# Performance work log

Hardware: AMD Instinct MI355X
Metric: run time of the kernel (lower is better)

Reference implementation:

```python
import jax, jax.numpy as jnp
import numpy as np

N_NODES = 100000
N_EDGES = 1600000
IN_DIM = 128
HID = 64
OUT_DIM = 3


def _glorot(key, shape):
    fan_in, fan_out = shape[0], shape[1]
    std = (2.0 / (fan_in + fan_out)) ** 0.5
    return jax.random.normal(key, shape, jnp.float32) * std


def setup_inputs() -> dict:
    key = jax.random.key(0)
    ks = jax.random.split(key, 12)
    x = jax.random.normal(ks[0], (N_NODES, IN_DIM), jnp.float32)
    edge_index = jax.random.randint(ks[1], (2, N_EDGES), 0, N_NODES, dtype=jnp.int32)
    return {
        "x": x,
        "edge_index": edge_index,
        "W1": _glorot(ks[2], (IN_DIM, HID)), "b1": jnp.zeros((HID,), jnp.float32),
        "W2": _glorot(ks[3], (HID, HID)), "b2": jnp.zeros((HID,), jnp.float32),
        "W3": _glorot(ks[4], (HID, HID)), "b3": jnp.zeros((HID,), jnp.float32),
        "W4": _glorot(ks[5], (HID, HID // 2)), "b4": jnp.zeros((HID // 2,), jnp.float32),
        "Wh": _glorot(ks[6], (HID // 2, OUT_DIM)), "bh": jnp.zeros((OUT_DIM,), jnp.float32),
    }


def reference(x, edge_index, W1, b1, W2, b2, W3, b3, W4, b4, Wh, bh):
    n = x.shape[0]
    self_loops = jnp.arange(n, dtype=edge_index.dtype)
    src = jnp.concatenate([edge_index[0], self_loops])  # message sources j
    dst = jnp.concatenate([edge_index[1], self_loops])  # aggregation targets i
    # symmetric GCN normalization with self-loops: deg over targets (unit edge weights)
    deg = jax.ops.segment_sum(jnp.ones_like(dst, jnp.float32), dst, num_segments=n)
    dinv = jnp.where(deg > 0, jax.lax.rsqrt(deg), 0.0)
    norm = dinv[src] * dinv[dst]  # [E+N]

    def gcn(h, W, b):
        h = h @ W  # transform first (PyG GCNConv order)
        agg = jax.ops.segment_sum(h[src] * norm[:, None], dst, num_segments=n)
        return agg + b

    h = jax.nn.relu(gcn(x, W1, b1))   # dropout is identity in eval mode
    h = jax.nn.relu(gcn(h, W2, b2))
    h = jax.nn.relu(gcn(h, W3, b3))
    h = jax.nn.relu(gcn(h, W4, b4))
    return h @ Wh + bh  # [N, 3]
```

## Files before the change

kernel.cpp:

```cpp
#include <hip/hip_runtime.h>
#include <hip/hip_bf16.h>
#include <hip/hip_fp16.h>
#include <cstdint>


#define MAXD 512
#define EB   8192
#define PADSLACK 2048

typedef _Float16 half8v __attribute__((ext_vector_type(8)));
typedef _Float16 half2v __attribute__((ext_vector_type(2)));
typedef float    float4v __attribute__((ext_vector_type(4)));

#if defined(__has_builtin)
#if __has_builtin(__builtin_amdgcn_fdot2)
#define HAVE_FDOT2 1
#endif
#endif

__device__ __forceinline__ float fdot2f(half2v a, half2v b, float c) {
#ifdef HAVE_FDOT2
    return __builtin_amdgcn_fdot2(a, b, c, false);
#else
    return c + (float)a[0] * (float)b[0] + (float)a[1] * (float)b[1];
#endif
}

__device__ __forceinline__ void digit_base_scan(const int* __restrict__ totals,
                                                int ND, int* pairs, int* cbs) {
    const int t = threadIdx.x;
    const int e0 = 2 * t, e1 = 2 * t + 1;
    int v0 = (e0 < ND) ? totals[e0] : 0;
    int v1 = (e1 < ND) ? totals[e1] : 0;
    pairs[t] = v0 + v1;
    __syncthreads();
    for (int off = 1; off < 256; off <<= 1) {
        int x = (t >= off) ? pairs[t - off] : 0;
        __syncthreads();
        pairs[t] += x;
        __syncthreads();
    }
    int ep = pairs[t] - v0 - v1;
    cbs[e0] = ep;
    cbs[e1] = ep + v0;
    __syncthreads();
}

__device__ __forceinline__ void hist_body(const int* __restrict__ ei,
                                          int* __restrict__ histM, int E, int b) {
    __shared__ int hist[MAXD];
    const int tid = threadIdx.x;
    hist[tid] = 0; hist[tid + 256] = 0;
    __syncthreads();
    const int base = b * EB;
#pragma unroll 2
    for (int it = 0; it < EB / 256; it += 4) {
        int d[4]; bool ok[4];
#pragma unroll
        for (int u = 0; u < 4; ++u) {
            int e = base + (it + u) * 256 + tid;
            ok[u] = e < E;
            d[u] = ok[u] ? ei[E + e] : 0;
        }
#pragma unroll
        for (int u = 0; u < 4; ++u)
            if (ok[u]) atomicAdd(&hist[d[u] >> 8], 1);
    }
    __syncthreads();
    histM[(size_t)b * MAXD + tid] = hist[tid];
    histM[(size_t)b * MAXD + tid + 256] = hist[tid + 256];
}

__global__ __launch_bounds__(256) void scan_digits_k(int* __restrict__ histM,
                                                     int* __restrict__ totals,
                                                     int NBLK) {
    __shared__ int s[256];
    const int t = threadIdx.x, dg = blockIdx.x;
    int v = (t < NBLK) ? histM[(size_t)t * MAXD + dg] : 0;
    s[t] = v;
    __syncthreads();
    for (int off = 1; off < 256; off <<= 1) {
        int x = (t >= off) ? s[t - off] : 0;
        __syncthreads();
        s[t] += x;
        __syncthreads();
    }
    if (t < NBLK) histM[(size_t)t * MAXD + dg] = s[t] - v;
    if (t == 255) totals[dg] = s[255];
}

__device__ __forceinline__ void gemm1_mfma_body(const float* __restrict__ X,
                                                const float* __restrict__ W,
                                                __half* __restrict__ Aout,
                                                int n, int bx) {
    __shared__ _Float16 WT[64][136];
    const int t = threadIdx.x;
#pragma unroll
    for (int p = 0; p < 8; ++p) {
        int f4 = t + p * 256;
        int k  = f4 >> 4;
        int o  = (f4 & 15) * 4;
        float4 v = reinterpret_cast<const float4*>(W)[f4];
        WT[o + 0][k] = (_Float16)v.x;
        WT[o + 1][k] = (_Float16)v.y;
        WT[o + 2][k] = (_Float16)v.z;
        WT[o + 3][k] = (_Float16)v.w;
    }
    __syncthreads();

    const int lane = t & 63;
    const int wv   = t >> 6;
    const int m16  = lane & 15;
    const int quad = lane >> 4;
    const int r0   = bx * 64 + wv * 16;
    int ra = r0 + m16; if (ra >= n) ra = n - 1;

    const float4* xrow = reinterpret_cast<const float4*>(X + (size_t)ra * 128);
    half8v a[4];
#pragma unroll
    for (int h = 0; h < 4; ++h) {
        int f0 = (h * 32 + quad * 8) >> 2;
        float4 v0 = xrow[f0];
        float4 v1 = xrow[f0 + 1];
        a[h][0] = (_Float16)v0.x; a[h][1] = (_Float16)v0.y;
        a[h][2] = (_Float16)v0.z; a[h][3] = (_Float16)v0.w;
        a[h][4] = (_Float16)v1.x; a[h][5] = (_Float16)v1.y;
        a[h][6] = (_Float16)v1.z; a[h][7] = (_Float16)v1.w;
    }
#pragma unroll
    for (int tt = 0; tt < 4; ++tt) {
        const half8v* wt = reinterpret_cast<const half8v*>(&WT[tt * 16 + m16][0]);
        float4v z = {0.f, 0.f, 0.f, 0.f};
#pragma unroll
        for (int h = 0; h < 4; ++h)
            z = __builtin_amdgcn_mfma_f32_16x16x32_f16(a[h], wt[h * 4 + quad], z, 0, 0, 0);
#pragma unroll
        for (int reg = 0; reg < 4; ++reg) {
            int row = r0 + quad * 4 + reg;
            if (row < n)
                Aout[(size_t)row * 64 + tt * 16 + m16] = __float2half_rn(z[reg]);
        }
    }
}

__device__ __forceinline__ void pack_body(const int* __restrict__ ei,
                                          const int* __restrict__ histM,
                                          const int* __restrict__ totals,
                                          int* __restrict__ packed,
                                          int E, int ND, int b) {
    __shared__ int pairs[256];
    __shared__ int cbs[MAXD];
    __shared__ int cur[MAXD];
    const int tid = threadIdx.x;
    digit_base_scan(totals, ND, pairs, cbs);
    for (int t = tid; t < ND; t += 256)
        cur[t] = cbs[t] + histM[(size_t)b * MAXD + t];
    __syncthreads();
    const int base = b * EB;
    for (int it = 0; it < EB / 256; it += 4) {
        int s[4], d[4]; bool ok[4];
#pragma unroll
        for (int u = 0; u < 4; ++u) {
            int e = base + (it + u) * 256 + tid;
            ok[u] = e < E;
            if (ok[u]) { s[u] = ei[e]; d[u] = ei[E + e]; }
        }
#pragma unroll
        for (int u = 0; u < 4; ++u) {
            if (ok[u]) {
                int pos = atomicAdd(&cur[d[u] >> 8], 1);
                packed[pos] = (s[u] << 8) | (d[u] & 255);
            }
        }
    }
}

__global__ __launch_bounds__(256) void hist_gemm1_k(
    const int* __restrict__ ei, int* __restrict__ histM, int E,
    const float* __restrict__ x, const float* __restrict__ W1,
    __half* __restrict__ A1, int n, int NH) {
    const int bx = blockIdx.x;
    if (bx < NH) hist_body(ei, histM, E, bx);
    else         gemm1_mfma_body(x, W1, A1, n, bx - NH);
}

__global__ __launch_bounds__(256) void pack_gemm1_k(
    const int* __restrict__ ei, const int* __restrict__ histM,
    const int* __restrict__ totals, int* __restrict__ packed,
    const float* __restrict__ x, const float* __restrict__ W1,
    __half* __restrict__ A1, int n, int E, int ND, int NPB, int G1) {
    const int bx = blockIdx.x;
    if (bx < NPB) pack_body(ei, histM, totals, packed, E, ND, bx);
    else          gemm1_mfma_body(x, W1, A1, n, G1 + bx - NPB);
}

__global__ __launch_bounds__(256) void bucket_k(const int* __restrict__ packed,
                                                const int* __restrict__ totals,
                                                int ND,
                                                int* __restrict__ col,
                                                int4* __restrict__ rpc,
                                                float* __restrict__ dinv,
                                                const __half* __restrict__ Araw,
                                                __half* __restrict__ Th, int n) {
    __shared__ int   pairs[256];
    __shared__ int   cbs[MAXD];
    __shared__ int   hist[256];
    __shared__ int   pref[256];
    __shared__ int   cur[256];
    __shared__ float dinv_l[256];

    const int tid = threadIdx.x;
    const int dg  = blockIdx.x;
    digit_base_scan(totals, ND, pairs, cbs);
    const int base  = cbs[dg];
    const int m     = totals[dg];
    const int basep = base + dg * PADSLACK;

    hist[tid] = 0;
    __syncthreads();
    for (int k0 = 0; k0 < m; k0 += 1024) {
        int v[4]; bool ok[4];
#pragma unroll
        for (int u = 0; u < 4; ++u) {
            int k = k0 + u * 256 + tid;
            ok[u] = k < m;
            v[u] = ok[u] ? packed[base + k] : 0;
        }
#pragma unroll
        for (int u = 0; u < 4; ++u)
            if (ok[u]) atomicAdd(&hist[v[u] & 255], 1);
    }
    __syncthreads();
    const int deg   = hist[tid];
    const int cnt_p = (deg + 8) & ~7;
    pref[tid] = cnt_p;
    __syncthreads();
    for (int off = 1; off < 256; off <<= 1) {
        int x = (tid >= off) ? pref[tid - off] : 0;
        __syncthreads();
        pref[tid] += x;
        __syncthreads();
    }
    const int rp = basep + pref[tid] - cnt_p;
    const float di = rsqrtf((float)(deg + 1));
    dinv_l[tid] = di;
    cur[tid] = rp + 1;
    const int d = dg * 256 + tid;
    if (d < n) {
        rpc[d]  = make_int4(rp, cnt_p, __float_as_int(di), 0);
        dinv[d] = di;
        col[rp] = d;
        for (int k = deg + 1; k < cnt_p; ++k) col[rp + k] = n;
    }
    __syncthreads();
    for (int k0 = 0; k0 < m; k0 += 1024) {
        int v[4]; bool ok[4];
#pragma unroll
        for (int u = 0; u < 4; ++u) {
            int k = k0 + u * 256 + tid;
            ok[u] = k < m;
            v[u] = ok[u] ? packed[base + k] : 0;
        }
#pragma unroll
        for (int u = 0; u < 4; ++u) {
            if (ok[u]) {
                int pos = atomicAdd(&cur[v[u] & 255], 1);
                col[pos] = v[u] >> 8;
            }
        }
    }
    const int r0 = dg * 256;
#pragma unroll 4
    for (int it = 0; it < 16; ++it) {
        int idx = it * 256 + tid;
        int rl  = idx >> 4;
        int r   = r0 + rl;
        if (r < n) {
            union { uint2 u; __half h[4]; } iv;
            iv.u = reinterpret_cast<const uint2*>(Araw)[(size_t)r * 16 + (idx & 15)];
            float dd = dinv_l[rl];
            union { ushort4 u; __half h[4]; } pk;
            pk.h[0] = __float2half_rn(__half2float(iv.h[0]) * dd);
            pk.h[1] = __float2half_rn(__half2float(iv.h[1]) * dd);
            pk.h[2] = __float2half_rn(__half2float(iv.h[2]) * dd);
            pk.h[3] = __float2half_rn(__half2float(iv.h[3]) * dd);
            reinterpret_cast<ushort4*>(Th)[(size_t)r * 16 + (idx & 15)] = pk.u;
        }
    }
    if (dg == 0 && tid < 16) {
        uint2 z; z.x = 0u; z.y = 0u;
        reinterpret_cast<uint2*>(Th)[(size_t)n * 16 + tid] = z;
    }
}

template <int OUT, int TSTRIDE>
__global__ __launch_bounds__(256) void gemm_mfma_k(
    const _Float16* __restrict__ H, const float* __restrict__ W,
    const float* __restrict__ dinv, _Float16* __restrict__ T, int n) {
    constexpr int NT = OUT / 16;
    const int lane = threadIdx.x & 63;
    const int m16  = lane & 15;
    const int quad = lane >> 4;
    const int wid  = (blockIdx.x * blockDim.x + threadIdx.x) >> 6;
    const int nw   = (gridDim.x * blockDim.x) >> 6;

    if constexpr (TSTRIDE == 32) {
        if (blockIdx.x == 0 && threadIdx.x < 8)
            reinterpret_cast<uint2*>(T)[(size_t)n * 8 + threadIdx.x] =
                make_uint2(0u, 0u);
    }

    half8v bfrag[NT][2];
#pragma unroll
    for (int t = 0; t < NT; ++t)
#pragma unroll
        for (int h = 0; h < 2; ++h)
#pragma unroll
            for (int j = 0; j < 8; ++j)
                bfrag[t][h][j] = (_Float16)W[(size_t)(h * 32 + quad * 8 + j) * OUT
                                             + t * 16 + m16];

    const int nblk = (n + 15) >> 4;
    for (int rb = wid; rb < nblk; rb += nw) {
        const int r0 = rb * 16;
        int ra = r0 + m16; if (ra >= n) ra = n - 1;
        const half8v* hrow = reinterpret_cast<const half8v*>(H + (size_t)ra * 64);
        half8v a0 = hrow[quad];
        half8v a1 = hrow[4 + quad];

        float4v dfr[NT];
#pragma unroll
        for (int t = 0; t < NT; ++t) {
            float4v z = {0.f, 0.f, 0.f, 0.f};
            z = __builtin_amdgcn_mfma_f32_16x16x32_f16(a0, bfrag[t][0], z, 0, 0, 0);
            z = __builtin_amdgcn_mfma_f32_16x16x32_f16(a1, bfrag[t][1], z, 0, 0, 0);
            dfr[t] = z;
        }
#pragma unroll
        for (int reg = 0; reg < 4; ++reg) {
            int row = r0 + quad * 4 + reg;
            if (row < n) {
                float di = dinv[row];
#pragma unroll
                for (int t = 0; t < NT; ++t)
                    T[(size_t)row * TSTRIDE + t * 16 + m16] =
                        (_Float16)(dfr[t][reg] * di);
            }
        }
    }
}

template <int NB, int LR>
__device__ __forceinline__ void gather_batch(int c_l, const uint2* __restrict__ T2,
                                             int q, int sw, float4& acc) {
    constexpr int NSW = 64 / LR;
    constexpr int GPE = 8 / NSW;
    constexpr int NV  = NB * GPE;
    const half2v s10 = {(_Float16)1.f, (_Float16)0.f};
    const half2v s01 = {(_Float16)0.f, (_Float16)1.f};
    uint2 v[NV];
#pragma unroll
    for (int g = 0; g < NB; ++g)
#pragma unroll
        for (int u = 0; u < GPE; ++u) {
            int cc = __shfl(c_l, g * 8 + u * NSW + sw, 64);
            v[g * GPE + u] = T2[(size_t)cc * LR + q];
        }
#pragma unroll
    for (int k = 0; k < NV; ++k) {
        union { uint2 uu; half2v h[2]; } cv; cv.uu = v[k];
        acc.x = fdot2f(cv.h[0], s10, acc.x);
        acc.y = fdot2f(cv.h[0], s01, acc.y);
        acc.z = fdot2f(cv.h[1], s10, acc.z);
        acc.w = fdot2f(cv.h[1], s01, acc.w);
    }
}

template <int LR, bool FUSE_HEAD>
__global__ __launch_bounds__(256, 8) void agg_k(const __half* __restrict__ T,
                                             const int4* __restrict__ rpc,
                                             const int* __restrict__ col,
                                             const float* __restrict__ bias,
                                             void* __restrict__ O, int n,
                                             const float* __restrict__ Wh,
                                             const float* __restrict__ bh) {
    constexpr int NSW = 64 / LR;
    constexpr int GPE = 8 / NSW;
    const int lane = threadIdx.x & 63;
    const int q    = lane % LR;
    const int sw   = lane / LR;
    const int wid  = (blockIdx.x * blockDim.x + threadIdx.x) >> 6;
    const int nw   = (gridDim.x * blockDim.x) >> 6;
    if (wid >= n) return;

    const uint2* __restrict__ T2 = reinterpret_cast<const uint2*>(T);
    const float4 b4 = reinterpret_cast<const float4*>(bias)[q];

    float wh[12]; float bh0 = 0.f, bh1 = 0.f, bh2 = 0.f;
    if constexpr (FUSE_HEAD) {
#pragma unroll
        for (int j = 0; j < 12; ++j) wh[j] = Wh[4 * q * 3 + j];
        bh0 = bh[0]; bh1 = bh[1]; bh2 = bh[2];
    }

    int ib = wid + nw; if (ib >= n) ib = n - 1;
    int4 rc_a = rpc[wid];
    int4 rc_b = rpc[ib];
    int  c_a  = col[rc_a.x + lane];

    for (int i = wid; i < n; i += nw) {
        int ic = i + 2 * nw; if (ic >= n) ic = n - 1;
        int4 rc_c = rpc[ic];
        int  c_nx = col[rc_b.x + lane];

        const int   cnt   = rc_a.y;
        const int   start = rc_a.x;
        const float di    = __int_as_float(rc_a.z);

        float4 acc = make_float4(0.f, 0.f, 0.f, 0.f);
        if (cnt <= 64) {
            switch (cnt >> 3) {
                case 1: gather_batch<1, LR>(c_a, T2, q, sw, acc); break;
                case 2: gather_batch<2, LR>(c_a, T2, q, sw, acc); break;
                case 3: gather_batch<3, LR>(c_a, T2, q, sw, acc); break;
                case 4: gather_batch<4, LR>(c_a, T2, q, sw, acc); break;
                case 5: gather_batch<5, LR>(c_a, T2, q, sw, acc); break;
                case 6: gather_batch<6, LR>(c_a, T2, q, sw, acc); break;
                case 7: gather_batch<7, LR>(c_a, T2, q, sw, acc); break;
                default: gather_batch<8, LR>(c_a, T2, q, sw, acc); break;
            }
        } else {
            const half2v s10 = {(_Float16)1.f, (_Float16)0.f};
            const half2v s01 = {(_Float16)0.f, (_Float16)1.f};
            for (int base = 0; base < cnt; base += 64) {
                const int m = min(64, cnt - base);
                int c_l = col[start + base + lane];
                for (int jg = 0; jg < m; jg += 8) {
                    int cc[GPE]; uint2 v[GPE];
#pragma unroll
                    for (int u = 0; u < GPE; ++u)
                        cc[u] = __shfl(c_l, jg + u * NSW + sw, 64);
#pragma unroll
                    for (int u = 0; u < GPE; ++u) v[u] = T2[(size_t)cc[u] * LR + q];
#pragma unroll
                    for (int u = 0; u < GPE; ++u) {
                        union { uint2 uu; half2v h[2]; } cv; cv.uu = v[u];
                        acc.x = fdot2f(cv.h[0], s10, acc.x);
                        acc.y = fdot2f(cv.h[0], s01, acc.y);
                        acc.z = fdot2f(cv.h[1], s10, acc.z);
                        acc.w = fdot2f(cv.h[1], s01, acc.w);
                    }
                }
            }
        }
#pragma unroll
        for (int off = LR; off < 64; off <<= 1) {
            acc.x += __shfl_xor(acc.x, off, 64);
            acc.y += __shfl_xor(acc.y, off, 64);
            acc.z += __shfl_xor(acc.z, off, 64);
            acc.w += __shfl_xor(acc.w, off, 64);
        }
        float4 h;
        h.x = fmaxf(fmaf(di, acc.x, b4.x), 0.f);
        h.y = fmaxf(fmaf(di, acc.y, b4.y), 0.f);
        h.z = fmaxf(fmaf(di, acc.z, b4.z), 0.f);
        h.w = fmaxf(fmaf(di, acc.w, b4.w), 0.f);
        if constexpr (!FUSE_HEAD) {
            if (sw == 0) {
                union { ushort4 u; __half hh[4]; } pk;
                pk.hh[0] = __float2half_rn(h.x);
                pk.hh[1] = __float2half_rn(h.y);
                pk.hh[2] = __float2half_rn(h.z);
                pk.hh[3] = __float2half_rn(h.w);
                ushort* base_p = (ushort*)O + (size_t)i * 64;
                *reinterpret_cast<ushort4*>(base_p + 4 * q) = pk.u;
            }
        } else {
            float* Of = (float*)O;
            float p0 = h.x * wh[0];
            float p1 = h.x * wh[1];
            float p2 = h.x * wh[2];
            p0 = fmaf(h.y, wh[3], p0);
            p1 = fmaf(h.y, wh[4], p1);
            p2 = fmaf(h.y, wh[5], p2);
            p0 = fmaf(h.z, wh[6], p0);
            p1 = fmaf(h.z, wh[7], p1);
            p2 = fmaf(h.z, wh[8], p2);
            p0 = fmaf(h.w, wh[9], p0);
            p1 = fmaf(h.w, wh[10], p1);
            p2 = fmaf(h.w, wh[11], p2);
#pragma unroll
            for (int off = 1; off < LR; off <<= 1) {
                p0 += __shfl_xor(p0, off, 64);
                p1 += __shfl_xor(p1, off, 64);
                p2 += __shfl_xor(p2, off, 64);
            }
            if (lane == 0) {
                Of[(size_t)i * 3 + 0] = p0 + bh0;
                Of[(size_t)i * 3 + 1] = p1 + bh1;
                Of[(size_t)i * 3 + 2] = p2 + bh2;
            }
        }
        rc_a = rc_b; rc_b = rc_c; c_a = c_nx;
    }
}

extern "C" void kernel_launch(void* const* d_in, const int* in_sizes, int n_in,
                              void* d_out, int out_size, void* d_ws, size_t ws_size,
                              hipStream_t stream) {
    const float* x  = (const float*)d_in[0];
    const int*   ei = (const int*)d_in[1];
    const float* W1 = (const float*)d_in[2];
    const float* b1 = (const float*)d_in[3];
    const float* W2 = (const float*)d_in[4];
    const float* b2 = (const float*)d_in[5];
    const float* W3 = (const float*)d_in[6];
    const float* b3 = (const float*)d_in[7];
    const float* W4 = (const float*)d_in[8];
    const float* b4 = (const float*)d_in[9];
    const float* Wh = (const float*)d_in[10];
    const float* bh = (const float*)d_in[11];
    float* out = (float*)d_out;

    const int n = in_sizes[0] / 128;
    const int E = in_sizes[1] / 2;
    const int ND   = (n + 255) / 256;
    const int NBLK = (E + EB - 1) / EB;

    char* ws = (char*)d_ws;
    auto alloc = [&](size_t bytes) {
        char* p = ws;
        ws += (bytes + 255) & ~(size_t)255;
        return p;
    };
    int*    histM  = (int*)alloc((size_t)NBLK * MAXD * 4);
    int*    totals = (int*)alloc((size_t)MAXD * 4);
    int*    packed = (int*)alloc((size_t)E * 4);
    int*    col    = (int*)alloc(((size_t)E + (size_t)ND * PADSLACK + 256) * 4);
    int4*   rpc    = (int4*)alloc((size_t)n * 16);
    float*  dinv   = (float*)alloc((size_t)n * 4);
    __half* bufA   = (__half*)alloc((size_t)n * 64 * 2);
    __half* bufH   = (__half*)alloc(((size_t)n + 1) * 64 * 2);
    __half* bufG   = bufA;

    dim3 blk(256);
    const int G  = (n + 63) / 64;
    const int G1 = G / 3;
    const int G2 = G - G1;
    const int agg_blocks = 2048;
    const int mfma_blocks = 640;

    hist_gemm1_k<<<dim3(NBLK + G1), blk, 0, stream>>>(ei, histM, E, x, W1, bufA, n, NBLK);
    scan_digits_k<<<dim3(ND), blk, 0, stream>>>(histM, totals, NBLK);
    pack_gemm1_k<<<dim3(NBLK + G2), blk, 0, stream>>>(ei, histM, totals, packed,
                                                      x, W1, bufA, n, E, ND, NBLK, G1);
    bucket_k<<<dim3(ND), blk, 0, stream>>>(packed, totals, ND, col, rpc,
                                           dinv, bufA, bufH, n);
    agg_k<16, false><<<dim3(agg_blocks), blk, 0, stream>>>(
        bufH, rpc, col, b1, bufG, n, nullptr, nullptr);
    gemm_mfma_k<64, 64><<<dim3(mfma_blocks), blk, 0, stream>>>(
        (const _Float16*)bufG, W2, dinv, (_Float16*)bufH, n);
    agg_k<16, false><<<dim3(agg_blocks), blk, 0, stream>>>(
        bufH, rpc, col, b2, bufG, n, nullptr, nullptr);
    gemm_mfma_k<64, 64><<<dim3(mfma_blocks), blk, 0, stream>>>(
        (const _Float16*)bufG, W3, dinv, (_Float16*)bufH, n);
    agg_k<16, false><<<dim3(agg_blocks), blk, 0, stream>>>(
        bufH, rpc, col, b3, bufG, n, nullptr, nullptr);
    gemm_mfma_k<32, 32><<<dim3(mfma_blocks), blk, 0, stream>>>(
        (const _Float16*)bufG, W4, dinv, (_Float16*)bufH, n);
    agg_k<8, true><<<dim3(agg_blocks), blk, 0, stream>>>(
        bufH, rpc, col, b4, out, n, Wh, bh);
}
```

Baseline: 352.0 us.

## Fuse aggregation with following MFMA GEMM into single per-layer kernel

Replaces the separate aggregation and MFMA GEMM kernels for layers 1-3 with one fused kernel. Each wave aggregates 16 nodes, applies bias, ReLU and fp16 rounding, stages the rows in LDS, then runs the 16x16x32 MFMA and writes the dinv-scaled output. This removes the global write and re-read of the intermediate hidden features and three kernel launches. In exchange it uses a fixed one-wave-per-16-nodes grid with no grid-stride load balancing, serial per-node gathers within a wave, and LDS usage that may lower occupancy.

```diff
diff --git a/kernel.cpp b/kernel.cpp
--- a/kernel.cpp
+++ b/kernel.cpp
@@ -293,63 +293,6 @@
     }
 }
 
-template <int OUT, int TSTRIDE>
-__global__ __launch_bounds__(256) void gemm_mfma_k(
-    const _Float16* __restrict__ H, const float* __restrict__ W,
-    const float* __restrict__ dinv, _Float16* __restrict__ T, int n) {
-    constexpr int NT = OUT / 16;
-    const int lane = threadIdx.x & 63;
-    const int m16  = lane & 15;
-    const int quad = lane >> 4;
-    const int wid  = (blockIdx.x * blockDim.x + threadIdx.x) >> 6;
-    const int nw   = (gridDim.x * blockDim.x) >> 6;
-
-    if constexpr (TSTRIDE == 32) {
-        if (blockIdx.x == 0 && threadIdx.x < 8)
-            reinterpret_cast<uint2*>(T)[(size_t)n * 8 + threadIdx.x] =
-                make_uint2(0u, 0u);
-    }
-
-    half8v bfrag[NT][2];
-#pragma unroll
-    for (int t = 0; t < NT; ++t)
-#pragma unroll
-        for (int h = 0; h < 2; ++h)
-#pragma unroll
-            for (int j = 0; j < 8; ++j)
-                bfrag[t][h][j] = (_Float16)W[(size_t)(h * 32 + quad * 8 + j) * OUT
-                                             + t * 16 + m16];
-
-    const int nblk = (n + 15) >> 4;
-    for (int rb = wid; rb < nblk; rb += nw) {
-        const int r0 = rb * 16;
-        int ra = r0 + m16; if (ra >= n) ra = n - 1;
-        const half8v* hrow = reinterpret_cast<const half8v*>(H + (size_t)ra * 64);
-        half8v a0 = hrow[quad];
-        half8v a1 = hrow[4 + quad];
-
-        float4v dfr[NT];
-#pragma unroll
-        for (int t = 0; t < NT; ++t) {
-            float4v z = {0.f, 0.f, 0.f, 0.f};
-            z = __builtin_amdgcn_mfma_f32_16x16x32_f16(a0, bfrag[t][0], z, 0, 0, 0);
-            z = __builtin_amdgcn_mfma_f32_16x16x32_f16(a1, bfrag[t][1], z, 0, 0, 0);
-            dfr[t] = z;
-        }
-#pragma unroll
-        for (int reg = 0; reg < 4; ++reg) {
-            int row = r0 + quad * 4 + reg;
-            if (row < n) {
-                float di = dinv[row];
-#pragma unroll
-                for (int t = 0; t < NT; ++t)
-                    T[(size_t)row * TSTRIDE + t * 16 + m16] =
-                        (_Float16)(dfr[t][reg] * di);
-            }
-        }
-    }
-}
-
 template <int NB, int LR>
 __device__ __forceinline__ void gather_batch(int c_l, const uint2* __restrict__ T2,
                                              int q, int sw, float4& acc) {
@@ -373,6 +316,144 @@
         acc.y = fdot2f(cv.h[0], s01, acc.y);
         acc.z = fdot2f(cv.h[1], s10, acc.z);
         acc.w = fdot2f(cv.h[1], s01, acc.w);
+    }
+}
+
+__device__ __forceinline__ void gather_node16(const int4& rc_a, int c_a,
+                                              const uint2* __restrict__ T2,
+                                              const int* __restrict__ col,
+                                              int lane, int q, int sw,
+                                              float4& acc) {
+    const int cnt   = rc_a.y;
+    const int start = rc_a.x;
+    if (cnt <= 64) {
+        switch (cnt >> 3) {
+            case 1: gather_batch<1, 16>(c_a, T2, q, sw, acc); break;
+            case 2: gather_batch<2, 16>(c_a, T2, q, sw, acc); break;
+            case 3: gather_batch<3, 16>(c_a, T2, q, sw, acc); break;
+            case 4: gather_batch<4, 16>(c_a, T2, q, sw, acc); break;
+            case 5: gather_batch<5, 16>(c_a, T2, q, sw, acc); break;
+            case 6: gather_batch<6, 16>(c_a, T2, q, sw, acc); break;
+            case 7: gather_batch<7, 16>(c_a, T2, q, sw, acc); break;
+            default: gather_batch<8, 16>(c_a, T2, q, sw, acc); break;
+        }
+    } else {
+        const half2v s10 = {(_Float16)1.f, (_Float16)0.f};
+        const half2v s01 = {(_Float16)0.f, (_Float16)1.f};
+        for (int base = 0; base < cnt; base += 64) {
+            const int m = min(64, cnt - base);
+            int c_l = col[start + base + lane];
+            for (int jg = 0; jg < m; jg += 8) {
+                int cc[2]; uint2 v[2];
+#pragma unroll
+                for (int u = 0; u < 2; ++u)
+                    cc[u] = __shfl(c_l, jg + u * 4 + sw, 64);
+#pragma unroll
+                for (int u = 0; u < 2; ++u) v[u] = T2[(size_t)cc[u] * 16 + q];
+#pragma unroll
+                for (int u = 0; u < 2; ++u) {
+                    union { uint2 uu; half2v h[2]; } cv; cv.uu = v[u];
+                    acc.x = fdot2f(cv.h[0], s10, acc.x);
+                    acc.y = fdot2f(cv.h[0], s01, acc.y);
+                    acc.z = fdot2f(cv.h[1], s10, acc.z);
+                    acc.w = fdot2f(cv.h[1], s01, acc.w);
+                }
+            }
+        }
+    }
+}
+
+template <int OUT, int TSTRIDE>
+__global__ __launch_bounds__(256, 6) void aggemm_k(
+    const __half* __restrict__ Tin, const int4* __restrict__ rpc,
+    const int* __restrict__ col, const float* __restrict__ bias,
+    const float* __restrict__ W, __half* __restrict__ Tout, int n) {
+    constexpr int NT = OUT / 16;
+    __shared__ _Float16 hrows[4][16 * 72];
+    __shared__ float    dinvb[4][16];
+
+    if (blockIdx.x == 0 && threadIdx.x < TSTRIDE / 4)
+        reinterpret_cast<uint2*>(Tout)[(size_t)n * (TSTRIDE / 4) + threadIdx.x] =
+            make_uint2(0u, 0u);
+
+    const int lane = threadIdx.x & 63;
+    const int wv   = threadIdx.x >> 6;
+    const int q    = lane & 15;
+    const int sw   = lane >> 4;
+    const int m16  = q;
+    const int quad = sw;
+    const int wid  = (blockIdx.x * blockDim.x + threadIdx.x) >> 6;
+    const int base = wid * 16;
+    if (base >= n) return;
+
+    const uint2* __restrict__ T2 = reinterpret_cast<const uint2*>(Tin);
+    const float4 b4 = reinterpret_cast<const float4*>(bias)[q];
+
+    half8v bfrag[NT][2];
+#pragma unroll
+    for (int t = 0; t < NT; ++t)
+#pragma unroll
+        for (int h = 0; h < 2; ++h)
+#pragma unroll
+            for (int j = 0; j < 8; ++j)
+                bfrag[t][h][j] = (_Float16)W[(size_t)(h * 32 + quad * 8 + j) * OUT
+                                             + t * 16 + m16];
+
+    int i1 = base + 1; if (i1 >= n) i1 = n - 1;
+    int4 rc_a = rpc[base];
+    int4 rc_b = rpc[i1];
+    int  c_a  = col[rc_a.x + lane];
+
+#pragma unroll 2
+    for (int kb = 0; kb < 16; ++kb) {
+        int ic = base + kb + 2; if (ic >= n) ic = n - 1;
+        int4 rc_c = rpc[ic];
+        int  c_nx = col[rc_b.x + lane];
+
+        const float di = __int_as_float(rc_a.z);
+        float4 acc = make_float4(0.f, 0.f, 0.f, 0.f);
+        gather_node16(rc_a, c_a, T2, col, lane, q, sw, acc);
+#pragma unroll
+        for (int off = 16; off < 64; off <<= 1) {
+            acc.x += __shfl_xor(acc.x, off, 64);
+            acc.y += __shfl_xor(acc.y, off, 64);
+            acc.z += __shfl_xor(acc.z, off, 64);
+            acc.w += __shfl_xor(acc.w, off, 64);
+        }
+        float4 h;
+        h.x = fmaxf(fmaf(di, acc.x, b4.x), 0.f);
+        h.y = fmaxf(fmaf(di, acc.y, b4.y), 0.f);
+        h.z = fmaxf(fmaf(di, acc.z, b4.z), 0.f);
+        h.w = fmaxf(fmaf(di, acc.w, b4.w), 0.f);
+        if (sw == 0) {
+            union { ushort4 u; __half hh[4]; } pk;
+            pk.hh[0] = __float2half_rn(h.x);
+            pk.hh[1] = __float2half_rn(h.y);
+            pk.hh[2] = __float2half_rn(h.z);
+            pk.hh[3] = __float2half_rn(h.w);
+            *reinterpret_cast<ushort4*>(&hrows[wv][kb * 72 + 4 * q]) = pk.u;
+        }
+        if (lane == 0) dinvb[wv][kb] = di;
+        rc_a = rc_b; rc_b = rc_c; c_a = c_nx;
+    }
+
+    const _Float16* hl = &hrows[wv][0];
+    half8v a0 = *reinterpret_cast<const half8v*>(&hl[m16 * 72 + quad * 8]);
+    half8v a1 = *reinterpret_cast<const half8v*>(&hl[m16 * 72 + 32 + quad * 8]);
+#pragma unroll
+    for (int t = 0; t < NT; ++t) {
+        float4v z = {0.f, 0.f, 0.f, 0.f};
+        z = __builtin_amdgcn_mfma_f32_16x16x32_f16(a0, bfrag[t][0], z, 0, 0, 0);
+        z = __builtin_amdgcn_mfma_f32_16x16x32_f16(a1, bfrag[t][1], z, 0, 0, 0);
+#pragma unroll
+        for (int reg = 0; reg < 4; ++reg) {
+            int row = base + quad * 4 + reg;
+            if (row < n) {
+                float di2 = dinvb[wv][quad * 4 + reg];
+                Tout[(size_t)row * TSTRIDE + t * 16 + m16] =
+                    (_Float16)(z[reg] * di2);
+            }
+        }
     }
 }
 
@@ -540,34 +621,25 @@
     int4*   rpc    = (int4*)alloc((size_t)n * 16);
     float*  dinv   = (float*)alloc((size_t)n * 4);
     __half* bufA   = (__half*)alloc((size_t)n * 64 * 2);
-    __half* bufH   = (__half*)alloc(((size_t)n + 1) * 64 * 2);
-    __half* bufG   = bufA;
+    __half* T1     = (__half*)alloc(((size_t)n + 1) * 64 * 2);
+    __half* T2     = (__half*)alloc(((size_t)n + 1) * 64 * 2);
 
     dim3 blk(256);
     const int G  = (n + 63) / 64;
     const int G1 = G / 3;
     const int G2 = G - G1;
     const int agg_blocks = 2048;
-    const int mfma_blocks = 640;
+    const int agm_blocks = (n + 16 * 4 - 1) / (16 * 4);
 
     hist_gemm1_k<<<dim3(NBLK + G1), blk, 0, stream>>>(ei, histM, E, x, W1, bufA, n, NBLK);
     scan_digits_k<<<dim3(ND), blk, 0, stream>>>(histM, totals, NBLK);
     pack_gemm1_k<<<dim3(NBLK + G2), blk, 0, stream>>>(ei, histM, totals, packed,
                                                       x, W1, bufA, n, E, ND, NBLK, G1);
     bucket_k<<<dim3(ND), blk, 0, stream>>>(packed, totals, ND, col, rpc,
-                                           dinv, bufA, bufH, n);
-    agg_k<16, false><<<dim3(agg_blocks), blk, 0, stream>>>(
-        bufH, rpc, col, b1, bufG, n, nullptr, nullptr);
-    gemm_mfma_k<64, 64><<<dim3(mfma_blocks), blk, 0, stream>>>(
-        (const _Float16*)bufG, W2, dinv, (_Float16*)bufH, n);
-    agg_k<16, false><<<dim3(agg_blocks), blk, 0, stream>>>(
-        bufH, rpc, col, b2, bufG, n, nullptr, nullptr);
-    gemm_mfma_k<64, 64><<<dim3(mfma_blocks), blk, 0, stream>>>(
-        (const _Float16*)bufG, W3, dinv, (_Float16*)bufH, n);
-    agg_k<16, false><<<dim3(agg_blocks), blk, 0, stream>>>(
-        bufH, rpc, col, b3, bufG, n, nullptr, nullptr);
-    gemm_mfma_k<32, 32><<<dim3(mfma_blocks), blk, 0, stream>>>(
-        (const _Float16*)bufG, W4, dinv, (_Float16*)bufH, n);
+                                           dinv, bufA, T1, n);
+    aggemm_k<64, 64><<<dim3(agm_blocks), blk, 0, stream>>>(T1, rpc, col, b1, W2, T2, n);
+    aggemm_k<64, 64><<<dim3(agm_blocks), blk, 0, stream>>>(T2, rpc, col, b2, W3, T1, n);
+    aggemm_k<32, 32><<<dim3(agm_blocks), blk, 0, stream>>>(T1, rpc, col, b3, W4, T2, n);
     agg_k<8, true><<<dim3(agg_blocks), blk, 0, stream>>>(
-        bufH, rpc, col, b4, out, n, Wh, bh);
-}
+        T2, rpc, col, b4, out, n, Wh, bh);
+}
```

After: 458.0 us. 30.1% more time.
